# Kernel optimization log

Measured on AMD Instinct MI355X. Metric: run time of the kernel, lower is better.

The kernel has to match this reference:

```python
import math
import jax
import jax.numpy as jnp
import numpy as np
from jax import lax

B_, L, D_MODEL = 2, 1024, 2048
D_STATE, D_CONV, EXPAND = 16, 4, 2
D_INNER = EXPAND * D_MODEL          # 4096
DT_RANK = math.ceil(D_MODEL / 16)   # 128


def setup_inputs() -> dict:
    key = jax.random.key(0)
    ks = jax.random.split(key, 8)
    hidden_states = jax.random.normal(ks[0], (B_, L, D_MODEL), jnp.float32)
    in_proj_w = jax.random.normal(ks[1], (2 * D_INNER, D_MODEL), jnp.float32) * (D_MODEL ** -0.5)
    conv_w = jax.random.normal(ks[2], (D_INNER, D_CONV), jnp.float32) * (D_CONV ** -0.5)
    conv_b = jnp.zeros((D_INNER,), jnp.float32)
    x_proj_w = jax.random.normal(ks[3], (DT_RANK + 2 * D_STATE, D_INNER), jnp.float32) * (D_INNER ** -0.5)
    dt_std = DT_RANK ** -0.5
    dt_proj_w = jax.random.uniform(ks[4], (D_INNER, DT_RANK), jnp.float32, minval=-dt_std, maxval=dt_std)
    # dt bias init: softplus^{-1} of dt sampled log-uniform in [1e-3, 1e-1]
    dt = jnp.exp(jax.random.uniform(ks[5], (D_INNER,), jnp.float32)
                 * (math.log(0.1) - math.log(0.001)) + math.log(0.001))
    dt = jnp.clip(dt, 1e-4)
    dt_proj_b = dt + jnp.log(-jnp.expm1(-dt))
    A_log = jnp.log(jnp.broadcast_to(jnp.arange(1, D_STATE + 1, dtype=jnp.float32), (D_INNER, D_STATE)))
    D = jnp.ones((D_INNER,), jnp.float32)
    out_proj_w = jax.random.normal(ks[6], (D_MODEL, D_INNER), jnp.float32) * (D_INNER ** -0.5)
    return {
        'hidden_states': hidden_states, 'in_proj_w': in_proj_w,
        'conv_w': conv_w, 'conv_b': conv_b, 'x_proj_w': x_proj_w,
        'dt_proj_w': dt_proj_w, 'dt_proj_b': dt_proj_b,
        'A_log': A_log, 'D': D, 'out_proj_w': out_proj_w,
    }


def _silu(v):
    return v * jax.nn.sigmoid(v)


def _mamba_forward(hidden_states, in_proj_w, conv_w, conv_b, x_proj_w,
                   dt_proj_w, dt_proj_b, A_log, D, out_proj_w):
    b, l, _ = hidden_states.shape
    # in_proj: (b,l,d_model) -> (b, 2*d_inner, l)
    xz = jnp.einsum('bld,ed->bel', hidden_states, in_proj_w)
    x, z = xz[:, :D_INNER, :], xz[:, D_INNER:, :]
    A = -jnp.exp(A_log.astype(jnp.float32))  # (d_inner, d_state)
    # causal depthwise conv1d + SiLU
    xp = jnp.pad(x, ((0, 0), (0, 0), (D_CONV - 1, 0)))
    x = lax.conv_general_dilated(
        xp, conv_w[:, None, :], window_strides=(1,), padding='VALID',
        dimension_numbers=('NCH', 'OIH', 'NCH'), feature_group_count=D_INNER)
    x = _silu(x + conv_b[None, :, None])  # (b, d_inner, l)
    # x_proj -> dt, B, C
    x_dbl = jnp.einsum('bdl,kd->blk', x, x_proj_w)  # (b,l,dt_rank+2n)
    dt_lo = x_dbl[..., :DT_RANK]
    Bmat = x_dbl[..., DT_RANK:DT_RANK + D_STATE]          # (b,l,n)
    Cmat = x_dbl[..., DT_RANK + D_STATE:]                 # (b,l,n)
    delta = jax.nn.softplus(jnp.einsum('blr,dr->bld', dt_lo, dt_proj_w)
                            + dt_proj_b.astype(jnp.float32))  # (b,l,d)
    xt = jnp.transpose(x, (2, 0, 1))       # (l,b,d)
    dl = jnp.transpose(delta, (1, 0, 2))   # (l,b,d)
    Bl = jnp.transpose(Bmat, (1, 0, 2))    # (l,b,n)
    Cl = jnp.transpose(Cmat, (1, 0, 2))    # (l,b,n)

    def step(h, inp):
        d_t, B_t, C_t, x_t = inp
        dA = jnp.exp(d_t[..., None] * A)                       # (b,d,n)
        h = h * dA + d_t[..., None] * B_t[:, None, :] * x_t[..., None]
        y_t = jnp.sum(h * C_t[:, None, :], axis=-1)            # (b,d)
        return h, y_t

    h0 = jnp.zeros((b, D_INNER, D_STATE), jnp.float32)
    _, ys = lax.scan(step, h0, (dl, Bl, Cl, xt))  # ys: (l,b,d)
    y = jnp.transpose(ys, (1, 0, 2))              # (b,l,d)
    y = y + jnp.transpose(x, (0, 2, 1)) * D[None, None, :]
    y = y * _silu(jnp.transpose(z, (0, 2, 1)))
    out = jnp.einsum('bld,ed->ble', y, out_proj_w)  # (b,l,d_model)
    return out


def reference(hidden_states, in_proj_w, conv_w, conv_b, x_proj_w,
              dt_proj_w, dt_proj_b, A_log, D, out_proj_w):
    return _mamba_forward(hidden_states, in_proj_w, conv_w, conv_b, x_proj_w,
                          dt_proj_w, dt_proj_b, A_log, D, out_proj_w)
```

## Files before the change

### kernel.cpp

```cpp
#include <hip/hip_runtime.h>
#include <hip/hip_bf16.h>
#include <stdint.h>

#define BB 2
#define LL 1024
#define DMODEL 2048
#define DINNER 4096
#define DSTATE 16
#define DTRANK 128
#define XDBL_LD 256
#define CHUNK 64
#define NCH (LL / CHUNK)

typedef unsigned short ushort;
using short8 = __attribute__((ext_vector_type(8))) short;
using f32x4  = __attribute__((ext_vector_type(4))) float;
using us4    = __attribute__((ext_vector_type(4))) ushort;

__device__ __forceinline__ float bf2f(ushort u) {
    union { uint32_t i; float f; } v; v.i = ((uint32_t)u) << 16; return v.f;
}
__device__ __forceinline__ ushort f2bf(float f) {
    union { float f; uint32_t i; } v; v.f = f;
    uint32_t lsb = (v.i >> 16) & 1u;
    uint32_t r = v.i + 0x7FFFu + lsb;
    return (ushort)(r >> 16);
}

__device__ __forceinline__ void glds16(const ushort* g, ushort* l) {
    __builtin_amdgcn_global_load_lds(
        (const __attribute__((address_space(1))) void*)g,
        (__attribute__((address_space(3))) void*)l,
        16, 0, 0);
}

__global__ __launch_bounds__(256) void k_cvt(
    const float4* __restrict__ hidden, const float4* __restrict__ inproj,
    const float4* __restrict__ dtw, const float4* __restrict__ outp,
    const float4* __restrict__ xproj,
    us4* __restrict__ hid_h, us4* __restrict__ inp_h, us4* __restrict__ dtp_h,
    us4* __restrict__ outp_h, us4* __restrict__ xpp)
{
    long i = (long)blockIdx.x * 256 + threadIdx.x;
    const float4* src; us4* dst; long j;
    if (i < 1048576)      { src = hidden; dst = hid_h;  j = i; }
    else if (i < 5242880) { src = inproj; dst = inp_h;  j = i - 1048576; }
    else if (i < 5373952) { src = dtw;    dst = dtp_h;  j = i - 5242880; }
    else if (i < 7471104) { src = outp;   dst = outp_h; j = i - 5373952; }
    else {
        j = i - 7471104; dst = xpp;
        if (j >= 163840) { us4 z = {0, 0, 0, 0}; dst[j] = z; return; }
        src = xproj;
    }
    float4 v = src[j];
    us4 o; o.x = f2bf(v.x); o.y = f2bf(v.y); o.z = f2bf(v.z); o.w = f2bf(v.w);
    dst[j] = o;
}

template <int EPI, bool WF, bool WH>
__device__ __forceinline__ void gemm_body(
    const ushort* __restrict__ A, int lda,
    const ushort* __restrict__ Bm, int ldb,
    float* __restrict__ Cf, ushort* __restrict__ Ch, int ldc,
    int K, const float* __restrict__ bias)
{
    __shared__ __align__(16) ushort sA[128 * 64];
    __shared__ __align__(16) ushort sB[128 * 64];

    const int tid  = threadIdx.x;
    const int lane = tid & 63;
    const int wave = tid >> 6;
    const int wr = wave >> 1, wc = wave & 1;

    const int NT = gridDim.x, MT = gridDim.y;
    int mt, nt;
    if ((NT & 7) == 0) {
        int lin   = blockIdx.y * NT + blockIdx.x;
        int strip = NT >> 3;
        int xcd   = lin & 7;
        int idx   = lin >> 3;
        nt = xcd * strip + (idx % strip);
        mt = idx / strip;
    } else { mt = blockIdx.y; nt = blockIdx.x; }
    const long m0 = (long)mt * 128;
    const long n0 = (long)nt * 128;

    const long zoff = (long)blockIdx.z;
    A  += zoff * (long)K;
    Bm += zoff * (long)K;
    const long Mrows = (long)MT * 128;
    if (WF) Cf += zoff * Mrows * (long)ldc;
    if (WH) Ch += zoff * Mrows * (long)ldc;

    f32x4 acc[4][4] = {};

    const int lrow = lane & 15;
    const int q    = lane >> 4;

    const int sr  = tid >> 3;
    const int scb = (tid & 7) ^ (sr & 7);
    const int sc  = scb << 3;
    const ushort* Ag = A  + (m0 + sr) * (long)lda + sc;
    const ushort* Bg = Bm + (n0 + sr) * (long)ldb + sc;
    ushort* lA = sA + tid * 8;
    ushort* lB = sB + tid * 8;

    for (int k0 = 0; k0 < K; k0 += 64) {
        __syncthreads();
        #pragma unroll
        for (int c = 0; c < 4; ++c) {
            glds16(Ag + (c * 32) * (long)lda + k0, lA + c * 2048);
            glds16(Bg + (c * 32) * (long)ldb + k0, lB + c * 2048);
        }
        __syncthreads();

        #pragma unroll
        for (int ks = 0; ks < 2; ++ks) {
            const int off = (((ks * 4 + q) ^ (lrow & 7)) << 3);
            short8 af[4], bf[4];
            #pragma unroll
            for (int i = 0; i < 4; ++i)
                af[i] = *(const short8*)&sA[(wr * 64 + i * 16 + lrow) * 64 + off];
            #pragma unroll
            for (int j = 0; j < 4; ++j)
                bf[j] = *(const short8*)&sB[(wc * 64 + j * 16 + lrow) * 64 + off];

            #pragma unroll
            for (int i = 0; i < 4; ++i)
                #pragma unroll
                for (int j = 0; j < 4; ++j)
                    acc[i][j] = __builtin_amdgcn_mfma_f32_16x16x32_bf16(
                        af[i], bf[j], acc[i][j], 0, 0, 0);
        }
    }

    const int r0 = q * 4;
    const int c0 = lane & 15;
    #pragma unroll
    for (int i = 0; i < 4; ++i) {
        #pragma unroll
        for (int j = 0; j < 4; ++j) {
            long col = n0 + wc * 64 + j * 16 + c0;
            float bv = 0.f;
            if (EPI == 1) bv = bias[col];
            #pragma unroll
            for (int r = 0; r < 4; ++r) {
                long row = m0 + wr * 64 + i * 16 + r0 + r;
                float v = acc[i][j][r];
                if (EPI == 1) {
                    v += bv;
                    v = (v > 20.f) ? v : log1pf(__expf(v));
                }
                long idx = row * (long)ldc + col;
                if (WF) Cf[idx] = v;
                if (WH) Ch[idx] = f2bf(v);
            }
        }
    }
}

__global__ __launch_bounds__(256) void k_inproj(
    const ushort* A, int lda, const ushort* Bm, int ldb,
    ushort* Ch, int ldc, int K)
{
    gemm_body<0, false, true>(A, lda, Bm, ldb, nullptr, Ch, ldc, K, nullptr);
}

__global__ __launch_bounds__(256) void k_outproj(
    const ushort* A, int lda, const ushort* Bm, int ldb,
    float* Cf, int ldc, int K)
{
    gemm_body<0, true, false>(A, lda, Bm, ldb, Cf, nullptr, ldc, K, nullptr);
}

__global__ __launch_bounds__(256) void k_xdbl(
    const ushort* __restrict__ A, int lda,
    const ushort* __restrict__ Bm, int ldb,
    float* __restrict__ Cf, int ldc, int Kz)
{
    const int tid  = threadIdx.x;
    const int lane = tid & 63;
    const int w    = tid >> 6;
    const int lrow = lane & 15;
    const int q    = lane >> 4;
    const long m0 = (long)blockIdx.y * 64 + w * 16;
    const long n0 = (long)blockIdx.x * 16;
    const long z  = blockIdx.z;

    const ushort* Ap = A  + (m0 + lrow) * (long)lda + z * Kz + q * 8;
    const ushort* Bp = Bm + (n0 + lrow) * (long)ldb + z * Kz + q * 8;

    f32x4 acc = {};
    for (int k0 = 0; k0 < Kz; k0 += 128) {
        #pragma unroll
        for (int u = 0; u < 4; ++u) {
            short8 af = *(const short8*)(Ap + k0 + u * 32);
            short8 bf = *(const short8*)(Bp + k0 + u * 32);
            acc = __builtin_amdgcn_mfma_f32_16x16x32_bf16(af, bf, acc, 0, 0, 0);
        }
    }

    float* Cz = Cf + z * (long)(BB * LL) * ldc;
    #pragma unroll
    for (int r = 0; r < 4; ++r)
        Cz[(m0 + q * 4 + r) * (long)ldc + n0 + lrow] = acc[r];
}

__global__ __launch_bounds__(256) void k_delta(
    const ushort* __restrict__ A,
    const ushort* __restrict__ Bm,
    const float* __restrict__ bias,
    ushort* __restrict__ Ch)
{
    const int tid  = threadIdx.x;
    const int lane = tid & 63;
    const int w    = tid >> 6;
    const int lrow = lane & 15;
    const int q    = lane >> 4;
    const long m0 = (long)blockIdx.y * 64 + w * 16;
    const long n0 = (long)blockIdx.x * 64;

    const ushort* Ap = A  + (m0 + lrow) * (long)XDBL_LD + q * 8;
    const ushort* Bp = Bm + (n0 + lrow) * (long)DTRANK + q * 8;

    f32x4 acc[4] = {};
    #pragma unroll
    for (int ks = 0; ks < 4; ++ks) {
        short8 af = *(const short8*)(Ap + ks * 32);
        #pragma unroll
        for (int j = 0; j < 4; ++j) {
            short8 bf = *(const short8*)(Bp + j * 16 * DTRANK + ks * 32);
            acc[j] = __builtin_amdgcn_mfma_f32_16x16x32_bf16(af, bf, acc[j], 0, 0, 0);
        }
    }

    #pragma unroll
    for (int j = 0; j < 4; ++j) {
        long col = n0 + j * 16 + lrow;
        float bv = bias[col];
        #pragma unroll
        for (int r = 0; r < 4; ++r) {
            float v = acc[j][r] + bv;
            v = (v > 20.f) ? v : log1pf(__expf(v));
            Ch[(m0 + q * 4 + r) * (long)DINNER + col] = f2bf(v);
        }
    }
}

__global__ __launch_bounds__(256) void k_xdbl_red(
    const float4* __restrict__ parts, float4* __restrict__ outF,
    us4* __restrict__ outH)
{
    int i = blockIdx.x * 256 + threadIdx.x;
    if (i >= 131072) return;
    float4 s = parts[i];
    #pragma unroll
    for (int z = 1; z < 4; ++z) {
        float4 v = parts[(long)z * 131072 + i];
        s.x += v.x; s.y += v.y; s.z += v.z; s.w += v.w;
    }
    outF[i] = s;
    us4 o; o.x = f2bf(s.x); o.y = f2bf(s.y); o.z = f2bf(s.z); o.w = f2bf(s.w);
    outH[i] = o;
}

__global__ __launch_bounds__(256) void k_out_red(
    const float4* __restrict__ parts, float4* __restrict__ outF)
{
    int i = blockIdx.x * 256 + threadIdx.x;
    if (i >= 1048576) return;
    float4 a = parts[i];
    float4 b = parts[1048576L + i];
    a.x += b.x; a.y += b.y; a.z += b.z; a.w += b.w;
    outF[i] = a;
}

__global__ __launch_bounds__(256) void k_conv(
    const ushort* __restrict__ xz,
    const float* __restrict__ cw,
    const float* __restrict__ cb,
    ushort* __restrict__ xc)
{
    int gid = blockIdx.x * 256 + threadIdx.x;
    int d  = gid & (DINNER - 1);
    int rl = gid >> 12;
    int l  = rl & (LL - 1);
    float acc = cb[d];
    #pragma unroll
    for (int j = 0; j < 4; ++j) {
        int li = l - 3 + j;
        if (li >= 0)
            acc += cw[d * 4 + j] * bf2f(xz[(long)(rl - 3 + j) * 8192 + d]);
    }
    float s = acc / (1.f + __expf(-acc));
    xc[gid] = f2bf(s);
}

__global__ __launch_bounds__(256) void k_scan1(
    const ushort* __restrict__ delta,
    const ushort* __restrict__ xc,
    const float*  __restrict__ xdbl,
    const float*  __restrict__ A_log,
    float* __restrict__ Hbuf,
    float* __restrict__ sumdt_buf)
{
    __shared__ float sB[CHUNK * 16];
    const int tid = threadIdx.x;
    const int k = blockIdx.y, b = blockIdx.z;
    const int d = blockIdx.x * 256 + tid;
    const int row0 = b * LL + k * CHUNK;

    #pragma unroll
    for (int i = 0; i < 4; ++i) {
        int idx = i * 256 + tid;
        sB[idx] = xdbl[(long)(row0 + (idx >> 4)) * XDBL_LD + DTRANK + (idx & 15)];
    }
    __syncthreads();

    float A[DSTATE];
    const float4* Ap = (const float4*)(A_log + d * DSTATE);
    #pragma unroll
    for (int i = 0; i < 4; ++i) {
        float4 v = Ap[i];
        A[i*4+0] = -__expf(v.x); A[i*4+1] = -__expf(v.y);
        A[i*4+2] = -__expf(v.z); A[i*4+3] = -__expf(v.w);
    }

    float H[DSTATE];
    #pragma unroll
    for (int s = 0; s < DSTATE; ++s) H[s] = 0.f;
    float sumdt = 0.f;

    for (int t = 0; t < CHUNK; ++t) {
        const long row = row0 + t;
        const float dt = bf2f(delta[row * DINNER + d]);
        const float xv = bf2f(xc[row * DINNER + d]);
        const float dx = dt * xv;
        sumdt += dt;
        #pragma unroll
        for (int s = 0; s < DSTATE; ++s) {
            float dA = __expf(dt * A[s]);
            H[s] = H[s] * dA + dx * sB[t * 16 + s];
        }
    }

    const long o = ((long)(b * NCH + k) * DINNER + d) * DSTATE;
    float4* Ho = (float4*)(Hbuf + o);
    #pragma unroll
    for (int i = 0; i < 4; ++i) {
        float4 v; v.x = H[i*4+0]; v.y = H[i*4+1]; v.z = H[i*4+2]; v.w = H[i*4+3];
        Ho[i] = v;
    }
    sumdt_buf[(b * NCH + k) * DINNER + d] = sumdt;
}

__global__ __launch_bounds__(256) void k_scan2(
    const float* __restrict__ A_log,
    const float* __restrict__ sumdt_buf,
    float* __restrict__ Hbuf)
{
    int gid = blockIdx.x * 256 + threadIdx.x;
    int b = gid >> 16;
    int rem = gid & 65535;
    int d = rem >> 4, s = rem & 15;
    float A = -__expf(A_log[d * DSTATE + s]);
    float h = 0.f;
    for (int k = 0; k < NCH; ++k) {
        long idx = ((long)(b * NCH + k) * DINNER + d) * DSTATE + s;
        float Hk = Hbuf[idx];
        float sd = sumdt_buf[(b * NCH + k) * DINNER + d];
        Hbuf[idx] = h;
        h = h * __expf(A * sd) + Hk;
    }
}

__global__ __launch_bounds__(256) void k_scan3(
    const ushort* __restrict__ delta,
    const ushort* __restrict__ xc,
    const float*  __restrict__ xdbl,
    const ushort* __restrict__ xz,
    const float*  __restrict__ A_log,
    const float*  __restrict__ Dp,
    const float*  __restrict__ hin,
    ushort* __restrict__ y)
{
    __shared__ float sBC[CHUNK * 32];
    const int tid = threadIdx.x;
    const int k = blockIdx.y, b = blockIdx.z;
    const int d = blockIdx.x * 256 + tid;
    const int row0 = b * LL + k * CHUNK;

    #pragma unroll
    for (int i = 0; i < 8; ++i) {
        int idx = i * 256 + tid;
        sBC[idx] = xdbl[(long)(row0 + (idx >> 5)) * XDBL_LD + DTRANK + (idx & 31)];
    }
    __syncthreads();

    float A[DSTATE];
    const float4* Ap = (const float4*)(A_log + d * DSTATE);
    #pragma unroll
    for (int i = 0; i < 4; ++i) {
        float4 v = Ap[i];
        A[i*4+0] = -__expf(v.x); A[i*4+1] = -__expf(v.y);
        A[i*4+2] = -__expf(v.z); A[i*4+3] = -__expf(v.w);
    }
    const float Dd = Dp[d];

    float h[DSTATE];
    const float4* Hp = (const float4*)(hin + ((long)(b * NCH + k) * DINNER + d) * DSTATE);
    #pragma unroll
    for (int i = 0; i < 4; ++i) {
        float4 v = Hp[i];
        h[i*4+0] = v.x; h[i*4+1] = v.y; h[i*4+2] = v.z; h[i*4+3] = v.w;
    }

    for (int t = 0; t < CHUNK; ++t) {
        const long row = row0 + t;
        const float dt = bf2f(delta[row * DINNER + d]);
        const float xv = bf2f(xc[row * DINNER + d]);
        const float dx = dt * xv;
        float yt = 0.f;
        #pragma unroll
        for (int s = 0; s < DSTATE; ++s) {
            float dA = __expf(dt * A[s]);
            h[s] = h[s] * dA + dx * sBC[t * 32 + s];
            yt += h[s] * sBC[t * 32 + 16 + s];
        }
        yt += xv * Dd;
        const float zv = bf2f(xz[row * 8192 + DINNER + d]);
        yt *= zv / (1.f + __expf(-zv));
        y[row * DINNER + d] = f2bf(yt);
    }
}

extern "C" void kernel_launch(void* const* d_in, const int* in_sizes, int n_in,
                              void* d_out, int out_size, void* d_ws, size_t ws_size,
                              hipStream_t stream)
{
    const float* hidden    = (const float*)d_in[0];
    const float* in_proj   = (const float*)d_in[1];
    const float* conv_w    = (const float*)d_in[2];
    const float* conv_b    = (const float*)d_in[3];
    const float* x_proj    = (const float*)d_in[4];
    const float* dt_proj_w = (const float*)d_in[5];
    const float* dt_proj_b = (const float*)d_in[6];
    const float* A_log     = (const float*)d_in[7];
    const float* Dp        = (const float*)d_in[8];
    const float* out_proj  = (const float*)d_in[9];
    float* out = (float*)d_out;

    char* ws = (char*)d_ws;
    ushort* xz_h    = (ushort*)(ws);
    ushort* xc      = (ushort*)(ws + 33554432);
    ushort* xpp     = (ushort*)(ws + 50331648);
    float*  xdbl    = (float*)(ws + 52428800);
    ushort* xdblh   = (ushort*)(ws + 54525952);
    ushort* delta_h = (ushort*)(ws + 55574528);
    ushort* yb      = (ushort*)(ws + 72351744);
    ushort* hid_h   = (ushort*)(ws + 89128960);
    ushort* inp_h   = (ushort*)(ws + 97517568);
    float*  parts   = (float*)(ws + 97517568);
    float*  Hbuf    = (float*)(ws + 97517568);
    float*  sumdt   = (float*)(ws + 105906176);
    ushort* dtp_h   = (ushort*)(ws + 131072000);
    ushort* outp_h  = (ushort*)(ws + 132120576);
    float*  parts2  = (float*)(ws);

    const int M = BB * LL;

    k_cvt<<<30208, 256, 0, stream>>>(
        (const float4*)hidden, (const float4*)in_proj, (const float4*)dt_proj_w,
        (const float4*)out_proj, (const float4*)x_proj,
        (us4*)hid_h, (us4*)inp_h, (us4*)dtp_h, (us4*)outp_h, (us4*)xpp);

    k_inproj<<<dim3(8192 / 128, M / 128), 256, 0, stream>>>(
        hid_h, DMODEL, inp_h, DMODEL, xz_h, 8192, DMODEL);

    k_conv<<<(M * DINNER) / 256, 256, 0, stream>>>(xz_h, conv_w, conv_b, xc);

    k_xdbl<<<dim3(XDBL_LD / 16, M / 64, 4), 256, 0, stream>>>(
        xc, DINNER, xpp, DINNER, parts, XDBL_LD, DINNER / 4);
    k_xdbl_red<<<131072 / 256, 256, 0, stream>>>(
        (const float4*)parts, (float4*)xdbl, (us4*)xdblh);

    k_delta<<<dim3(DINNER / 64, M / 64), 256, 0, stream>>>(
        xdblh, dtp_h, dt_proj_b, delta_h);

    k_scan1<<<dim3(DINNER / 256, NCH, BB), 256, 0, stream>>>(
        delta_h, xc, xdbl, A_log, Hbuf, sumdt);
    k_scan2<<<(BB * DINNER * DSTATE) / 256, 256, 0, stream>>>(
        A_log, sumdt, Hbuf);
    k_scan3<<<dim3(DINNER / 256, NCH, BB), 256, 0, stream>>>(
        delta_h, xc, xdbl, xz_h, A_log, Dp, Hbuf, yb);

    k_outproj<<<dim3(DMODEL / 128, M / 128, 2), 256, 0, stream>>>(
        yb, DINNER, outp_h, DINNER, parts2, DMODEL, DINNER / 2);
    k_out_red<<<1048576 / 256, 256, 0, stream>>>(
        (const float4*)parts2, (float4*)out);
}
```

Baseline: 509.5 us.

## Fold split-K reductions into consumers and use atomic accumulation for out_proj

Removes the two separate split-K reduction kernels. The x_proj partial sums are now reduced on the fly inside k_delta, k_scan1 and k_scan3, each of which reads all four partials. The out_proj split-K halves now atomically add into a zeroed output buffer after a memset. This cuts two kernel launches and one full write/read round trip of the reduced buffers, at the cost of redundant partial-sum reads, fp32 atomics on the output, and a memset.

Result: slower. 544.2 us (+6.8%).

```diff
diff --git a/kernel.cpp b/kernel.cpp
--- a/kernel.cpp
+++ b/kernel.cpp
@@ -11,6 +11,7 @@
 #define XDBL_LD 256
 #define CHUNK 64
 #define NCH (LL / CHUNK)
+#define PZ4 524288
 
 typedef unsigned short ushort;
 using short8 = __attribute__((ext_vector_type(8))) short;
@@ -57,12 +58,11 @@
     dst[j] = o;
 }
 
-template <int EPI, bool WF, bool WH>
+template <bool WF, bool WH, bool ATOM>
 __device__ __forceinline__ void gemm_body(
     const ushort* __restrict__ A, int lda,
     const ushort* __restrict__ Bm, int ldb,
-    float* __restrict__ Cf, ushort* __restrict__ Ch, int ldc,
-    int K, const float* __restrict__ bias)
+    float* __restrict__ Cf, ushort* __restrict__ Ch, int ldc, int K)
 {
     __shared__ __align__(16) ushort sA[128 * 64];
     __shared__ __align__(16) ushort sB[128 * 64];
@@ -88,9 +88,6 @@
     const long zoff = (long)blockIdx.z;
     A  += zoff * (long)K;
     Bm += zoff * (long)K;
-    const long Mrows = (long)MT * 128;
-    if (WF) Cf += zoff * Mrows * (long)ldc;
-    if (WH) Ch += zoff * Mrows * (long)ldc;
 
     f32x4 acc[4][4] = {};
 
@@ -141,19 +138,14 @@
         #pragma unroll
         for (int j = 0; j < 4; ++j) {
             long col = n0 + wc * 64 + j * 16 + c0;
-            float bv = 0.f;
-            if (EPI == 1) bv = bias[col];
             #pragma unroll
             for (int r = 0; r < 4; ++r) {
                 long row = m0 + wr * 64 + i * 16 + r0 + r;
                 float v = acc[i][j][r];
-                if (EPI == 1) {
-                    v += bv;
-                    v = (v > 20.f) ? v : log1pf(__expf(v));
-                }
                 long idx = row * (long)ldc + col;
-                if (WF) Cf[idx] = v;
-                if (WH) Ch[idx] = f2bf(v);
+                if (ATOM)      atomicAdd(&Cf[idx], v);
+                else if (WF)   Cf[idx] = v;
+                if (WH)        Ch[idx] = f2bf(v);
             }
         }
     }
@@ -163,14 +155,14 @@
     const ushort* A, int lda, const ushort* Bm, int ldb,
     ushort* Ch, int ldc, int K)
 {
-    gemm_body<0, false, true>(A, lda, Bm, ldb, nullptr, Ch, ldc, K, nullptr);
+    gemm_body<false, true, false>(A, lda, Bm, ldb, nullptr, Ch, ldc, K);
 }
 
 __global__ __launch_bounds__(256) void k_outproj(
     const ushort* A, int lda, const ushort* Bm, int ldb,
     float* Cf, int ldc, int K)
 {
-    gemm_body<0, true, false>(A, lda, Bm, ldb, Cf, nullptr, ldc, K, nullptr);
+    gemm_body<true, false, true>(A, lda, Bm, ldb, Cf, nullptr, ldc, K);
 }
 
 __global__ __launch_bounds__(256) void k_xdbl(
@@ -200,14 +192,14 @@
         }
     }
 
-    float* Cz = Cf + z * (long)(BB * LL) * ldc;
+    float* Cz = Cf + z * (long)PZ4;
     #pragma unroll
     for (int r = 0; r < 4; ++r)
         Cz[(m0 + q * 4 + r) * (long)ldc + n0 + lrow] = acc[r];
 }
 
 __global__ __launch_bounds__(256) void k_delta(
-    const ushort* __restrict__ A,
+    const float* __restrict__ parts,
     const ushort* __restrict__ Bm,
     const float* __restrict__ bias,
     ushort* __restrict__ Ch)
@@ -220,13 +212,23 @@
     const long m0 = (long)blockIdx.y * 64 + w * 16;
     const long n0 = (long)blockIdx.x * 64;
 
-    const ushort* Ap = A  + (m0 + lrow) * (long)XDBL_LD + q * 8;
+    const float*  Ap = parts + (m0 + lrow) * (long)XDBL_LD + q * 8;
     const ushort* Bp = Bm + (n0 + lrow) * (long)DTRANK + q * 8;
 
     f32x4 acc[4] = {};
     #pragma unroll
     for (int ks = 0; ks < 4; ++ks) {
-        short8 af = *(const short8*)(Ap + ks * 32);
+        float s[8] = {};
+        #pragma unroll
+        for (int z = 0; z < 4; ++z) {
+            float4 u0 = *(const float4*)(Ap + (long)z * PZ4 + ks * 32);
+            float4 u1 = *(const float4*)(Ap + (long)z * PZ4 + ks * 32 + 4);
+            s[0] += u0.x; s[1] += u0.y; s[2] += u0.z; s[3] += u0.w;
+            s[4] += u1.x; s[5] += u1.y; s[6] += u1.z; s[7] += u1.w;
+        }
+        short8 af;
+        #pragma unroll
+        for (int e = 0; e < 8; ++e) af[e] = (short)f2bf(s[e]);
         #pragma unroll
         for (int j = 0; j < 4; ++j) {
             short8 bf = *(const short8*)(Bp + j * 16 * DTRANK + ks * 32);
@@ -245,34 +247,6 @@
             Ch[(m0 + q * 4 + r) * (long)DINNER + col] = f2bf(v);
         }
     }
-}
-
-__global__ __launch_bounds__(256) void k_xdbl_red(
-    const float4* __restrict__ parts, float4* __restrict__ outF,
-    us4* __restrict__ outH)
-{
-    int i = blockIdx.x * 256 + threadIdx.x;
-    if (i >= 131072) return;
-    float4 s = parts[i];
-    #pragma unroll
-    for (int z = 1; z < 4; ++z) {
-        float4 v = parts[(long)z * 131072 + i];
-        s.x += v.x; s.y += v.y; s.z += v.z; s.w += v.w;
-    }
-    outF[i] = s;
-    us4 o; o.x = f2bf(s.x); o.y = f2bf(s.y); o.z = f2bf(s.z); o.w = f2bf(s.w);
-    outH[i] = o;
-}
-
-__global__ __launch_bounds__(256) void k_out_red(
-    const float4* __restrict__ parts, float4* __restrict__ outF)
-{
-    int i = blockIdx.x * 256 + threadIdx.x;
-    if (i >= 1048576) return;
-    float4 a = parts[i];
-    float4 b = parts[1048576L + i];
-    a.x += b.x; a.y += b.y; a.z += b.z; a.w += b.w;
-    outF[i] = a;
 }
 
 __global__ __launch_bounds__(256) void k_conv(
@@ -299,7 +273,7 @@
 __global__ __launch_bounds__(256) void k_scan1(
     const ushort* __restrict__ delta,
     const ushort* __restrict__ xc,
-    const float*  __restrict__ xdbl,
+    const float*  __restrict__ parts,
     const float*  __restrict__ A_log,
     float* __restrict__ Hbuf,
     float* __restrict__ sumdt_buf)
@@ -313,7 +287,8 @@
     #pragma unroll
     for (int i = 0; i < 4; ++i) {
         int idx = i * 256 + tid;
-        sB[idx] = xdbl[(long)(row0 + (idx >> 4)) * XDBL_LD + DTRANK + (idx & 15)];
+        const float* p = parts + (long)(row0 + (idx >> 4)) * XDBL_LD + DTRANK + (idx & 15);
+        sB[idx] = p[0] + p[PZ4] + p[2 * PZ4] + p[3 * PZ4];
     }
     __syncthreads();
 
@@ -377,7 +352,7 @@
 __global__ __launch_bounds__(256) void k_scan3(
     const ushort* __restrict__ delta,
     const ushort* __restrict__ xc,
-    const float*  __restrict__ xdbl,
+    const float*  __restrict__ parts,
     const ushort* __restrict__ xz,
     const float*  __restrict__ A_log,
     const float*  __restrict__ Dp,
@@ -393,7 +368,8 @@
     #pragma unroll
     for (int i = 0; i < 8; ++i) {
         int idx = i * 256 + tid;
-        sBC[idx] = xdbl[(long)(row0 + (idx >> 5)) * XDBL_LD + DTRANK + (idx & 31)];
+        const float* p = parts + (long)(row0 + (idx >> 5)) * XDBL_LD + DTRANK + (idx & 31);
+        sBC[idx] = p[0] + p[PZ4] + p[2 * PZ4] + p[3 * PZ4];
     }
     __syncthreads();
 
@@ -454,18 +430,15 @@
     ushort* xz_h    = (ushort*)(ws);
     ushort* xc      = (ushort*)(ws + 33554432);
     ushort* xpp     = (ushort*)(ws + 50331648);
-    float*  xdbl    = (float*)(ws + 52428800);
-    ushort* xdblh   = (ushort*)(ws + 54525952);
     ushort* delta_h = (ushort*)(ws + 55574528);
     ushort* yb      = (ushort*)(ws + 72351744);
     ushort* hid_h   = (ushort*)(ws + 89128960);
     ushort* inp_h   = (ushort*)(ws + 97517568);
     float*  parts   = (float*)(ws + 97517568);
-    float*  Hbuf    = (float*)(ws + 97517568);
-    float*  sumdt   = (float*)(ws + 105906176);
+    float*  Hbuf    = (float*)(ws + 105906176);
+    float*  sumdt   = (float*)(ws + 114294784);
     ushort* dtp_h   = (ushort*)(ws + 131072000);
     ushort* outp_h  = (ushort*)(ws + 132120576);
-    float*  parts2  = (float*)(ws);
 
     const int M = BB * LL;
 
@@ -481,21 +454,18 @@
 
     k_xdbl<<<dim3(XDBL_LD / 16, M / 64, 4), 256, 0, stream>>>(
         xc, DINNER, xpp, DINNER, parts, XDBL_LD, DINNER / 4);
-    k_xdbl_red<<<131072 / 256, 256, 0, stream>>>(
-        (const float4*)parts, (float4*)xdbl, (us4*)xdblh);
 
     k_delta<<<dim3(DINNER / 64, M / 64), 256, 0, stream>>>(
-        xdblh, dtp_h, dt_proj_b, delta_h);
+        parts, dtp_h, dt_proj_b, delta_h);
 
     k_scan1<<<dim3(DINNER / 256, NCH, BB), 256, 0, stream>>>(
-        delta_h, xc, xdbl, A_log, Hbuf, sumdt);
+        delta_h, xc, parts, A_log, Hbuf, sumdt);
     k_scan2<<<(BB * DINNER * DSTATE) / 256, 256, 0, stream>>>(
         A_log, sumdt, Hbuf);
     k_scan3<<<dim3(DINNER / 256, NCH, BB), 256, 0, stream>>>(
-        delta_h, xc, xdbl, xz_h, A_log, Dp, Hbuf, yb);
-
+        delta_h, xc, parts, xz_h, A_log, Dp, Hbuf, yb);
+
+    hipMemsetAsync(out, 0, (size_t)M * DMODEL * sizeof(float), stream);
     k_outproj<<<dim3(DMODEL / 128, M / 128, 2), 256, 0, stream>>>(
-        yb, DINNER, outp_h, DINNER, parts2, DMODEL, DINNER / 2);
-    k_out_red<<<1048576 / 256, 256, 0, stream>>>(
-        (const float4*)parts2, (float4*)out);
-}
+        yb, DINNER, outp_h, DINNER, out, DMODEL, DINNER / 2);
+}
```
